# Performance work log

Measured on AMD Instinct MI355X. Metric: run time of the kernel, lower is better.

## Reference

```python
import jax, jax.numpy as jnp
import numpy as np

B, N, C = 16, 577, 768
H = 12
D = C // H
HID = C // 2
TEMP_MIN, TEMP_MAX = 0.5, 3.0


def setup_inputs() -> dict:
    key = jax.random.key(0)
    ks = jax.random.split(key, 8)
    s = 0.02
    return {
        "x": jax.random.normal(ks[0], (B, N, C), dtype=jnp.float32),
        "qkv_w": jax.random.normal(ks[1], (C, 3 * C), dtype=jnp.float32) * s,
        "proj_w": jax.random.normal(ks[2], (C, C), dtype=jnp.float32) * s,
        "proj_b": jnp.zeros((C,), dtype=jnp.float32),
        "t_w1": jax.random.normal(ks[3], (C, HID), dtype=jnp.float32) * s,
        "t_b1": jnp.zeros((HID,), dtype=jnp.float32),
        "t_w2": jax.random.normal(ks[4], (HID, 1), dtype=jnp.float32) * s,
        "t_b2": jnp.zeros((1,), dtype=jnp.float32),
    }


def reference(x, qkv_w, proj_w, proj_b, t_w1, t_b1, t_w2, t_b2):
    b, n, c = x.shape
    scale = D ** -0.5
    # instance-wise temperature from CLS token: (B, 1)
    cls = x[:, 0]
    h = jax.nn.relu(cls @ t_w1 + t_b1)
    t_norm = jax.nn.sigmoid(h @ t_w2 + t_b2)
    temperature = TEMP_MIN + (TEMP_MAX - TEMP_MIN) * t_norm  # (B, 1)

    qkv = (x @ qkv_w).reshape(b, n, 3, H, D)
    q = qkv[:, :, 0].transpose(0, 2, 1, 3)  # (B, H, N, D)
    k = qkv[:, :, 1].transpose(0, 2, 1, 3)
    v = qkv[:, :, 2].transpose(0, 2, 1, 3)

    attn = jnp.einsum('bhqd,bhkd->bhqk', q, k) * scale
    attn = attn / temperature[:, :, None, None]  # (B,1,1,1) broadcast
    attn = jax.nn.softmax(attn, axis=-1)
    out = jnp.einsum('bhqk,bhkd->bhqd', attn, v)
    out = out.transpose(0, 2, 1, 3).reshape(b, n, c)
    return out @ proj_w + proj_b
```

## Files before the change

kernel.cpp:

```cpp
#include <hip/hip_runtime.h>
#include <hip/hip_bf16.h>
#include <stdint.h>

typedef unsigned short u16;
typedef unsigned int   u32;
typedef uint64_t       u64;

using f32x4  = __attribute__((ext_vector_type(4))) float;
using bf16x8 = __attribute__((ext_vector_type(8))) short;

__device__ __forceinline__ u16 f2bf(float f){
  u32 x = __builtin_bit_cast(u32, f);
  x = x + 0x7fffu + ((x >> 16) & 1u);
  return (u16)(x >> 16);
}

__device__ __forceinline__ void gload16(const void* g, void* l){
  __builtin_amdgcn_global_load_lds(
      (const __attribute__((address_space(1))) void*)g,
      (__attribute__((address_space(3))) void*)l, 16, 0, 0);
}

__device__ __forceinline__ bf16x8 mkfrag(uint2 h0, uint2 h1){
  union { bf16x8 v; u32 u[4]; } f;
  f.u[0]=h0.x; f.u[1]=h0.y; f.u[2]=h1.x; f.u[3]=h1.y;
  return f.v;
}

__global__ void convx(const float* __restrict__ in, u16* __restrict__ out, int n4){
  for (int i = blockIdx.x*256 + threadIdx.x; i < n4; i += gridDim.x*256){
    float4 v = ((const float4*)in)[i];
    ushort4 o;
    o.x = f2bf(v.x); o.y = f2bf(v.y); o.z = f2bf(v.z); o.w = f2bf(v.w);
    ((ushort4*)out)[i] = o;
  }
}

__global__ __launch_bounds__(256) void wtrans(const float* __restrict__ in,
                                              u16* __restrict__ out, int K, int N){
  __shared__ float tile[32][33];
  const int t = threadIdx.x;
  const int n0 = blockIdx.x*32, k0 = blockIdx.y*32;
  const int r = t >> 3, c4 = (t & 7)*4;
  const float4 v = *(const float4*)(in + (u64)(k0 + r)*N + n0 + c4);
  tile[r][c4+0]=v.x; tile[r][c4+1]=v.y; tile[r][c4+2]=v.z; tile[r][c4+3]=v.w;
  __syncthreads();
  ushort4 o;
  o.x = f2bf(tile[c4+0][r]); o.y = f2bf(tile[c4+1][r]);
  o.z = f2bf(tile[c4+2][r]); o.w = f2bf(tile[c4+3][r]);
  *(ushort4*)(out + (u64)(n0 + r)*K + k0 + c4) = o;
}

__global__ __launch_bounds__(384) void temp_kernel(
    const float* __restrict__ x, const float* __restrict__ w1,
    const float* __restrict__ b1, const float* __restrict__ w2,
    const float* __restrict__ b2, float* __restrict__ lsc){
  const int b = blockIdx.x, t = threadIdx.x;
  __shared__ float cls[768];
  __shared__ float part[6];
  const float* xr = x + (u64)b*577*768;
  cls[t] = xr[t]; cls[t+384] = xr[t+384];
  __syncthreads();
  float h0 = 0.f, h1 = 0.f, h2 = 0.f, h3 = 0.f;
  for (int i = 0; i < 768; i += 4){
    h0 = fmaf(cls[i+0], w1[(u64)(i+0)*384 + t], h0);
    h1 = fmaf(cls[i+1], w1[(u64)(i+1)*384 + t], h1);
    h2 = fmaf(cls[i+2], w1[(u64)(i+2)*384 + t], h2);
    h3 = fmaf(cls[i+3], w1[(u64)(i+3)*384 + t], h3);
  }
  float hacc = fmaxf((h0 + h1) + (h2 + h3) + b1[t], 0.f);
  float v = hacc * w2[t];
  #pragma unroll
  for (int off = 1; off < 64; off <<= 1) v += __shfl_xor(v, off);
  if ((t & 63) == 0) part[t >> 6] = v;
  __syncthreads();
  if (t == 0){
    float s2 = b2[0];
    for (int i = 0; i < 6; i++) s2 += part[i];
    float sig  = 1.f / (1.f + expf(-s2));
    float temp = 0.5f + 2.5f * sig;
    lsc[b] = 0.125f / temp;
  }
}

template<int OUTF>
__global__ __launch_bounds__(256, 2) void gemm_nt(
    const u16* __restrict__ A, const u16* __restrict__ Bm,
    void* __restrict__ Cout, const float* __restrict__ bias,
    const float* __restrict__ lsc, int M, int N){
  constexpr int K = 768;
  __shared__ u16 As[128*64];
  __shared__ u16 Bs[128*64];
  const int t = threadIdx.x, l = t & 63, w = t >> 6;
  const int bm = blockIdx.y*128, bn = blockIdx.x*128;
  const int wr = (w >> 1)*64, wc = (w & 1)*64;
  const int g = l >> 4, r16 = l & 15;

  f32x4 acc[4][4];
  #pragma unroll
  for (int i = 0; i < 4; i++)
    #pragma unroll
    for (int j = 0; j < 4; j++) acc[i][j] = (f32x4){0.f,0.f,0.f,0.f};

  const int srow = t >> 3;
  const int su   = (t & 7) ^ (srow & 7);
  const u16* gA[4]; const u16* gB[4];
  #pragma unroll
  for (int i = 0; i < 4; i++){
    int ra = bm + i*32 + srow; if (ra > M-1) ra = M-1;
    gA[i] = A  + (u64)ra*K + su*8;
    gB[i] = Bm + (u64)(bn + i*32 + srow)*K + su*8;
  }
  u16* lA = As + t*8;
  u16* lB = Bs + t*8;

  for (int kt = 0; kt < K; kt += 64){
    #pragma unroll
    for (int i = 0; i < 4; i++) gload16(gA[i] + kt, lA + i*2048);
    #pragma unroll
    for (int i = 0; i < 4; i++) gload16(gB[i] + kt, lB + i*2048);
    __syncthreads();
    #pragma unroll
    for (int s = 0; s < 2; s++){
      const int c   = s*4 + (g >> 1);
      const int off = (g & 1)*4;
      bf16x8 af[4], bfr[4];
      #pragma unroll
      for (int m = 0; m < 4; m++){
        const int R = wr + m*16 + r16;
        const int i1 = R*64 + ((c ^ (R & 7))*8) + off;
        af[m] = mkfrag(*(const uint2*)(As + i1), *(const uint2*)(As + (i1 ^ 16)));
      }
      #pragma unroll
      for (int n = 0; n < 4; n++){
        const int R = wc + n*16 + r16;
        const int i1 = R*64 + ((c ^ (R & 7))*8) + off;
        bfr[n] = mkfrag(*(const uint2*)(Bs + i1), *(const uint2*)(Bs + (i1 ^ 16)));
      }
      #pragma unroll
      for (int m = 0; m < 4; m++)
        #pragma unroll
        for (int n = 0; n < 4; n++)
          acc[m][n] = __builtin_amdgcn_mfma_f32_16x16x32_bf16(af[m], bfr[n], acc[m][n], 0, 0, 0);
    }
    __syncthreads();
  }
  const int row0 = bm + wr + g*4;
  const int col0 = bn + wc + r16;
  const bool isQ = (OUTF == 2) && (bn < 768);
  #pragma unroll
  for (int m = 0; m < 4; m++){
    #pragma unroll
    for (int rr = 0; rr < 4; rr++){
      const int row = row0 + m*16 + rr;
      if (row < M){
        float qs = 1.0f;
        if (isQ) qs = lsc[row/577];
        #pragma unroll
        for (int n = 0; n < 4; n++){
          const int col = col0 + n*16;
          const float v = acc[m][n][rr];
          if (OUTF == 1) ((float*)Cout)[(u64)row*N + col] = v + bias[col];
          else           ((u16*)Cout)[(u64)row*N + col]  = f2bf(v*qs);
        }
      }
    }
  }
}

__global__ __launch_bounds__(256, 2) void attn_kernel(
    const u16* __restrict__ qkv, u16* __restrict__ aout){
  const u32 lid  = blockIdx.x;
  const u32 orig = (lid & 7u)*240u + (lid >> 3);
  const int qt = orig % 10u;
  const u32 bh = orig / 10u;
  const int h  = bh % 12u;
  const int b  = bh / 12u;
  const int t = threadIdx.x, w = t >> 6, l = t & 63;
  const int g = l >> 4, r16 = l & 15;
  __shared__ u16 Ks[2][64*64];
  __shared__ u16 Vt[2][64*64];
  const u16* base = qkv + (u64)b*577*2304 + (u64)h*64;

  int qn = qt*64 + w*16 + r16; if (qn > 576) qn = 576;
  bf16x8 qf[2];
  {
    const u16* qr = base + (u64)qn*2304;
    #pragma unroll
    for (int s = 0; s < 2; s++)
      qf[s] = mkfrag(*(const uint2*)(qr + s*32 + g*4),
                     *(const uint2*)(qr + s*32 + g*4 + 16));
  }
  float m_run = -1e30f, l_run = 0.f;
  f32x4 oacc[4];
  #pragma unroll
  for (int i = 0; i < 4; i++) oacc[i] = (f32x4){0,0,0,0};

  const int srcb = (l & 48) | (((l >> 4) & 3)*4);

  const int srow = t >> 3;
  const int su   = (t & 7) ^ (srow & 7);
  const u16* pK = base + 768  + (u64)srow*2304 + su*8;
  const int kr0 = (t >> 3)*2;
  const u16* pV = base + 1536 + (u64)kr0*2304 + (t & 7)*8;
  u32 vtoff[8];
  #pragma unroll
  for (int j = 0; j < 8; j++){
    const int d = (t & 7)*8 + j;
    const int key = (d ^ (d >> 3)) & 7;
    vtoff[j] = d*64 + (((kr0 >> 3) ^ key)*8) + (kr0 & 7);
  }

  uint4 vr0, vr1;
  gload16(pK,            &Ks[0][0] + t*8);
  gload16(pK + 32*2304,  &Ks[0][0] + t*8 + 2048);
  vr0 = *(const uint4*)pV;
  vr1 = *(const uint4*)(pV + 2304);
  pK += 64*2304; pV += 64*2304;
  {
    const u16* e0 = (const u16*)&vr0;
    const u16* e1 = (const u16*)&vr1;
    #pragma unroll
    for (int j = 0; j < 8; j++)
      *(u32*)(&Vt[0][0] + vtoff[j]) = (u32)e0[j] | ((u32)e1[j] << 16);
  }
  __syncthreads();

  for (int kt = 0; kt < 9; kt++){
    const int cur = kt & 1, nb = cur ^ 1;
    u16* ksc = &Ks[cur][0];
    u16* vtc = &Vt[cur][0];
    if (kt < 8){
      gload16(pK,           &Ks[nb][0] + t*8);
      gload16(pK + 32*2304, &Ks[nb][0] + t*8 + 2048);
      vr0 = *(const uint4*)pV;
      vr1 = *(const uint4*)(pV + 2304);
      pK += 64*2304; pV += 64*2304;
    }

    f32x4 sacc[4];
    #pragma unroll
    for (int i = 0; i < 4; i++) sacc[i] = (f32x4){0,0,0,0};
    #pragma unroll
    for (int fn = 0; fn < 4; fn++){
      const int kr = fn*16 + r16;
      const int kk = kr & 7;
      const u16* rowp = ksc + kr*64 + (g & 1)*4;
      #pragma unroll
      for (int s = 0; s < 2; s++){
        const int b0 = (4*s + (g >> 1)) ^ kk;
        sacc[fn] = __builtin_amdgcn_mfma_f32_16x16x32_bf16(
            mkfrag(*(const uint2*)(rowp + b0*8), *(const uint2*)(rowp + (b0 ^ 2)*8)),
            qf[s], sacc[fn], 0, 0, 0);
      }
    }
    float mx = sacc[0][0];
    #pragma unroll
    for (int fn = 0; fn < 4; fn++)
      #pragma unroll
      for (int rr = 0; rr < 4; rr++) mx = fmaxf(mx, sacc[fn][rr]);
    mx = fmaxf(mx, __shfl_xor(mx, 16));
    mx = fmaxf(mx, __shfl_xor(mx, 32));
    if (!__all(mx - m_run <= 8.f)){
      const float nm = fmaxf(m_run, mx);
      const float corr = __expf(m_run - nm);
      l_run *= corr;
      float corrO[4];
      #pragma unroll
      for (int rr = 0; rr < 4; rr++) corrO[rr] = __shfl(corr, srcb + rr);
      #pragma unroll
      for (int df = 0; df < 4; df++)
        #pragma unroll
        for (int rr = 0; rr < 4; rr++) oacc[df][rr] *= corrO[rr];
      m_run = nm;
    }
    float pf[4][4];
    float rs = 0.f;
    #pragma unroll
    for (int fn = 0; fn < 4; fn++)
      #pragma unroll
      for (int rr = 0; rr < 4; rr++){
        const float p = __expf(sacc[fn][rr] - m_run);
        rs += p;
        pf[fn][rr] = p;
      }
    rs += __shfl_xor(rs, 16);
    rs += __shfl_xor(rs, 32);
    l_run += rs;
    #pragma unroll
    for (int s = 0; s < 2; s++){
      union { bf16x8 v; u32 u[4]; } pa;
      asm("v_cvt_pk_bf16_f32 %0, %1, %2" : "=v"(pa.u[0]) : "v"(pf[2*s][0]),   "v"(pf[2*s][1]));
      asm("v_cvt_pk_bf16_f32 %0, %1, %2" : "=v"(pa.u[1]) : "v"(pf[2*s][2]),   "v"(pf[2*s][3]));
      asm("v_cvt_pk_bf16_f32 %0, %1, %2" : "=v"(pa.u[2]) : "v"(pf[2*s+1][0]), "v"(pf[2*s+1][1]));
      asm("v_cvt_pk_bf16_f32 %0, %1, %2" : "=v"(pa.u[3]) : "v"(pf[2*s+1][2]), "v"(pf[2*s+1][3]));
      #pragma unroll
      for (int df = 0; df < 4; df++){
        const int vd = df*16 + r16;
        const int vk = (vd ^ (vd >> 3)) & 7;
        const u16* vrp = vtc + vd*64 + (g & 1)*4;
        const int c0 = (4*s + (g >> 1)) ^ vk;
        const bf16x8 vf = mkfrag(*(const uint2*)(vrp + c0*8),
                                 *(const uint2*)(vrp + (c0 ^ 2)*8));
        oacc[df] = __builtin_amdgcn_mfma_f32_16x16x32_bf16(pa.v, vf, oacc[df], 0, 0, 0);
      }
    }
    if (kt < 8){
      const u16* e0 = (const u16*)&vr0;
      const u16* e1 = (const u16*)&vr1;
      u16* vtn = &Vt[nb][0];
      #pragma unroll
      for (int j = 0; j < 8; j++)
        *(u32*)(vtn + vtoff[j]) = (u32)e0[j] | ((u32)e1[j] << 16);
      __syncthreads();
    }
  }

  {
    const u16* kr576 = base + 768 + (u64)576*2304;
    float s576 = 0.f;
    #pragma unroll
    for (int s = 0; s < 2; s++){
      const uint2 k0 = *(const uint2*)(kr576 + s*32 + g*4);
      const uint2 k1 = *(const uint2*)(kr576 + s*32 + g*4 + 16);
      union { bf16x8 v; u32 u[4]; } qq; qq.v = qf[s];
      const u32 ku[4] = {k0.x, k0.y, k1.x, k1.y};
      #pragma unroll
      for (int j = 0; j < 4; j++){
        const float ql = __builtin_bit_cast(float, qq.u[j] << 16);
        const float qh = __builtin_bit_cast(float, qq.u[j] & 0xffff0000u);
        const float kl = __builtin_bit_cast(float, ku[j] << 16);
        const float kh = __builtin_bit_cast(float, ku[j] & 0xffff0000u);
        s576 = fmaf(ql, kl, s576);
        s576 = fmaf(qh, kh, s576);
      }
    }
    s576 += __shfl_xor(s576, 16);
    s576 += __shfl_xor(s576, 32);
    if (!__all(s576 - m_run <= 8.f)){
      const float nm = fmaxf(m_run, s576);
      const float corr = __expf(m_run - nm);
      l_run *= corr;
      float corrO[4];
      #pragma unroll
      for (int rr = 0; rr < 4; rr++) corrO[rr] = __shfl(corr, srcb + rr);
      #pragma unroll
      for (int df = 0; df < 4; df++)
        #pragma unroll
        for (int rr = 0; rr < 4; rr++) oacc[df][rr] *= corrO[rr];
      m_run = nm;
    }
    const float p576 = __expf(s576 - m_run);
    l_run += p576;
    float pbr[4];
    #pragma unroll
    for (int rr = 0; rr < 4; rr++) pbr[rr] = __shfl(p576, srcb + rr);
    const u16* v576 = base + 1536 + (u64)576*2304;
    #pragma unroll
    for (int df = 0; df < 4; df++){
      const float vv = __builtin_bit_cast(float, (u32)v576[df*16 + r16] << 16);
      #pragma unroll
      for (int rr = 0; rr < 4; rr++)
        oacc[df][rr] = fmaf(pbr[rr], vv, oacc[df][rr]);
    }
  }

  float lO[4];
  #pragma unroll
  for (int rr = 0; rr < 4; rr++) lO[rr] = __shfl(l_run, srcb + rr);
  #pragma unroll
  for (int df = 0; df < 4; df++){
    const int d = df*16 + r16;
    #pragma unroll
    for (int rr = 0; rr < 4; rr++){
      const int n = qt*64 + w*16 + g*4 + rr;
      if (n <= 576){
        const float v = oacc[df][rr] / lO[rr];
        aout[(u64)(b*577 + n)*768 + h*64 + d] = f2bf(v);
      }
    }
  }
}

extern "C" void kernel_launch(void* const* d_in, const int* in_sizes, int n_in,
                              void* d_out, int out_size, void* d_ws, size_t ws_size,
                              hipStream_t stream){
  const float* x      = (const float*)d_in[0];
  const float* qkv_w  = (const float*)d_in[1];
  const float* proj_w = (const float*)d_in[2];
  const float* proj_b = (const float*)d_in[3];
  const float* t_w1   = (const float*)d_in[4];
  const float* t_b1   = (const float*)d_in[5];
  const float* t_w2   = (const float*)d_in[6];
  const float* t_b2   = (const float*)d_in[7];

  const u64 off_xb  = 256;
  const u64 off_qwT = off_xb  + 14180352ull;
  const u64 off_pwT = off_qwT + 3538944ull;
  const u64 off_qkv = off_pwT + 1179648ull;
  const u64 need    = off_qkv + 42541056ull;
  if (ws_size < need) return;

  char* ws  = (char*)d_ws;
  float* lsc = (float*)ws;
  u16* xb   = (u16*)(ws + off_xb);
  u16* qwT  = (u16*)(ws + off_qwT);
  u16* pwT  = (u16*)(ws + off_pwT);
  u16* qkv  = (u16*)(ws + off_qkv);
  u16* ao   = xb;

  convx<<<1024, 256, 0, stream>>>(x, xb, (16*577*768)/4);
  wtrans<<<dim3(2304/32, 768/32), 256, 0, stream>>>(qkv_w, qwT, 768, 2304);
  wtrans<<<dim3(768/32, 768/32), 256, 0, stream>>>(proj_w, pwT, 768, 768);
  temp_kernel<<<16, 384, 0, stream>>>(x, t_w1, t_b1, t_w2, t_b2, lsc);
  gemm_nt<2><<<dim3(2304/128, 73), 256, 0, stream>>>(xb, qwT, qkv, nullptr, lsc, 9232, 2304);
  attn_kernel<<<1920, 256, 0, stream>>>(qkv, ao);
  gemm_nt<1><<<dim3(768/128, 73), 256, 0, stream>>>(ao, pwT, d_out, proj_b, nullptr, 9232, 768);
}
```

Before: 238.3 us.

## Fuse prep kernels into one launch and remap GEMM tiles per XCD

Folds the x-to-bf16 conversion, the two weight transposes and the temperature MLP into a single prep kernel that dispatches on block index, cutting three kernel launches and their gaps. Separately, both GEMMs move to a 1D grid whose block ids are remapped so consecutive output tiles land on the same XCD, which should improve L2 reuse of the A/B panels. The temperature path now runs with 256 threads handling two hidden units each. The fused kernel carries the shared-memory footprint of every branch, and the temperature blocks are few and serial, so they may form a tail.

Result: faster. 232.9 us (-2.2%).

```diff
diff --git a/kernel.cpp b/kernel.cpp
--- a/kernel.cpp
+++ b/kernel.cpp
@@ -27,59 +27,75 @@
   return f.v;
 }
 
-__global__ void convx(const float* __restrict__ in, u16* __restrict__ out, int n4){
-  for (int i = blockIdx.x*256 + threadIdx.x; i < n4; i += gridDim.x*256){
-    float4 v = ((const float4*)in)[i];
+__global__ __launch_bounds__(256) void prep_kernel(
+    const float* __restrict__ x, const float* __restrict__ qkv_w,
+    const float* __restrict__ proj_w,
+    const float* __restrict__ t_w1, const float* __restrict__ t_b1,
+    const float* __restrict__ t_w2, const float* __restrict__ t_b2,
+    u16* __restrict__ xb, u16* __restrict__ qwT, u16* __restrict__ pwT,
+    float* __restrict__ lsc){
+  __shared__ float tile[32][33];
+  __shared__ float cls[768];
+  __shared__ float part[4];
+  const int bid = blockIdx.x, t = threadIdx.x;
+
+  if (bid < 1024){
+    const int n4 = 16*577*768/4;
+    for (int i = bid*256 + t; i < n4; i += 1024*256){
+      float4 v = ((const float4*)x)[i];
+      ushort4 o;
+      o.x = f2bf(v.x); o.y = f2bf(v.y); o.z = f2bf(v.z); o.w = f2bf(v.w);
+      ((ushort4*)xb)[i] = o;
+    }
+  } else if (bid < 3328){
+    const bool isQ = bid < 2752;
+    const int r    = isQ ? (bid - 1024) : (bid - 2752);
+    const int nbx  = isQ ? 72 : 24;
+    const int N    = isQ ? 2304 : 768;
+    const float* in = isQ ? qkv_w : proj_w;
+    u16* out        = isQ ? qwT   : pwT;
+    const int n0 = (r % nbx)*32, k0 = (r / nbx)*32;
+    const int rr = t >> 3, c4 = (t & 7)*4;
+    const float4 v = *(const float4*)(in + (u64)(k0 + rr)*N + n0 + c4);
+    tile[rr][c4+0]=v.x; tile[rr][c4+1]=v.y; tile[rr][c4+2]=v.z; tile[rr][c4+3]=v.w;
+    __syncthreads();
     ushort4 o;
-    o.x = f2bf(v.x); o.y = f2bf(v.y); o.z = f2bf(v.z); o.w = f2bf(v.w);
-    ((ushort4*)out)[i] = o;
-  }
-}
-
-__global__ __launch_bounds__(256) void wtrans(const float* __restrict__ in,
-                                              u16* __restrict__ out, int K, int N){
-  __shared__ float tile[32][33];
-  const int t = threadIdx.x;
-  const int n0 = blockIdx.x*32, k0 = blockIdx.y*32;
-  const int r = t >> 3, c4 = (t & 7)*4;
-  const float4 v = *(const float4*)(in + (u64)(k0 + r)*N + n0 + c4);
-  tile[r][c4+0]=v.x; tile[r][c4+1]=v.y; tile[r][c4+2]=v.z; tile[r][c4+3]=v.w;
-  __syncthreads();
-  ushort4 o;
-  o.x = f2bf(tile[c4+0][r]); o.y = f2bf(tile[c4+1][r]);
-  o.z = f2bf(tile[c4+2][r]); o.w = f2bf(tile[c4+3][r]);
-  *(ushort4*)(out + (u64)(n0 + r)*K + k0 + c4) = o;
-}
-
-__global__ __launch_bounds__(384) void temp_kernel(
-    const float* __restrict__ x, const float* __restrict__ w1,
-    const float* __restrict__ b1, const float* __restrict__ w2,
-    const float* __restrict__ b2, float* __restrict__ lsc){
-  const int b = blockIdx.x, t = threadIdx.x;
-  __shared__ float cls[768];
-  __shared__ float part[6];
-  const float* xr = x + (u64)b*577*768;
-  cls[t] = xr[t]; cls[t+384] = xr[t+384];
-  __syncthreads();
-  float h0 = 0.f, h1 = 0.f, h2 = 0.f, h3 = 0.f;
-  for (int i = 0; i < 768; i += 4){
-    h0 = fmaf(cls[i+0], w1[(u64)(i+0)*384 + t], h0);
-    h1 = fmaf(cls[i+1], w1[(u64)(i+1)*384 + t], h1);
-    h2 = fmaf(cls[i+2], w1[(u64)(i+2)*384 + t], h2);
-    h3 = fmaf(cls[i+3], w1[(u64)(i+3)*384 + t], h3);
-  }
-  float hacc = fmaxf((h0 + h1) + (h2 + h3) + b1[t], 0.f);
-  float v = hacc * w2[t];
-  #pragma unroll
-  for (int off = 1; off < 64; off <<= 1) v += __shfl_xor(v, off);
-  if ((t & 63) == 0) part[t >> 6] = v;
-  __syncthreads();
-  if (t == 0){
-    float s2 = b2[0];
-    for (int i = 0; i < 6; i++) s2 += part[i];
-    float sig  = 1.f / (1.f + expf(-s2));
-    float temp = 0.5f + 2.5f * sig;
-    lsc[b] = 0.125f / temp;
+    o.x = f2bf(tile[c4+0][rr]); o.y = f2bf(tile[c4+1][rr]);
+    o.z = f2bf(tile[c4+2][rr]); o.w = f2bf(tile[c4+3][rr]);
+    *(ushort4*)(out + (u64)(n0 + rr)*768 + k0 + c4) = o;
+  } else {
+    const int b = bid - 3328;
+    const float* xr = x + (u64)b*577*768;
+    cls[t] = xr[t]; cls[t+256] = xr[t+256]; cls[t+512] = xr[t+512];
+    __syncthreads();
+    float v = 0.f;
+    if (t < 192){
+      const int j = t*2;
+      float a0=0.f, a1=0.f, b0=0.f, b1=0.f;
+      for (int i = 0; i < 768; i += 2){
+        const float2 w0 = *(const float2*)(t_w1 + (u64)i*384 + j);
+        const float2 w1v = *(const float2*)(t_w1 + (u64)(i+1)*384 + j);
+        a0 = fmaf(cls[i],   w0.x,  a0);
+        b0 = fmaf(cls[i],   w0.y,  b0);
+        a1 = fmaf(cls[i+1], w1v.x, a1);
+        b1 = fmaf(cls[i+1], w1v.y, b1);
+      }
+      const float2 bb = *(const float2*)(t_b1 + j);
+      const float2 ww = *(const float2*)(t_w2 + j);
+      const float hA = fmaxf(a0 + a1 + bb.x, 0.f);
+      const float hB = fmaxf(b0 + b1 + bb.y, 0.f);
+      v = hA*ww.x + hB*ww.y;
+    }
+    #pragma unroll
+    for (int off = 1; off < 64; off <<= 1) v += __shfl_xor(v, off);
+    if ((t & 63) == 0) part[t >> 6] = v;
+    __syncthreads();
+    if (t == 0){
+      const float s2 = part[0] + part[1] + part[2] + part[3] + t_b2[0];
+      const float sig  = 1.f / (1.f + expf(-s2));
+      const float temp = 0.5f + 2.5f * sig;
+      lsc[b] = 0.125f / temp;
+    }
   }
 }
 
@@ -87,12 +103,16 @@
 __global__ __launch_bounds__(256, 2) void gemm_nt(
     const u16* __restrict__ A, const u16* __restrict__ Bm,
     void* __restrict__ Cout, const float* __restrict__ bias,
-    const float* __restrict__ lsc, int M, int N){
+    const float* __restrict__ lsc, int M, int N, int nbx){
   constexpr int K = 768;
   __shared__ u16 As[128*64];
   __shared__ u16 Bs[128*64];
   const int t = threadIdx.x, l = t & 63, w = t >> 6;
-  const int bm = blockIdx.y*128, bn = blockIdx.x*128;
+  const u32 nwg = gridDim.x;
+  const u32 qc = nwg >> 3, rc = nwg & 7;
+  const u32 xcd = blockIdx.x & 7, lin = blockIdx.x >> 3;
+  const u32 wg = (xcd < rc ? xcd*(qc+1) : rc*(qc+1) + (xcd-rc)*qc) + lin;
+  const int bm = (int)(wg / (u32)nbx)*128, bn = (int)(wg % (u32)nbx)*128;
   const int wr = (w >> 1)*64, wc = (w & 1)*64;
   const int g = l >> 4, r16 = l & 15;
 
@@ -409,11 +429,9 @@
   u16* qkv  = (u16*)(ws + off_qkv);
   u16* ao   = xb;
 
-  convx<<<1024, 256, 0, stream>>>(x, xb, (16*577*768)/4);
-  wtrans<<<dim3(2304/32, 768/32), 256, 0, stream>>>(qkv_w, qwT, 768, 2304);
-  wtrans<<<dim3(768/32, 768/32), 256, 0, stream>>>(proj_w, pwT, 768, 768);
-  temp_kernel<<<16, 384, 0, stream>>>(x, t_w1, t_b1, t_w2, t_b2, lsc);
-  gemm_nt<2><<<dim3(2304/128, 73), 256, 0, stream>>>(xb, qwT, qkv, nullptr, lsc, 9232, 2304);
+  prep_kernel<<<3344, 256, 0, stream>>>(x, qkv_w, proj_w, t_w1, t_b1, t_w2, t_b2,
+                                        xb, qwT, pwT, lsc);
+  gemm_nt<2><<<1314, 256, 0, stream>>>(xb, qwT, qkv, nullptr, lsc, 9232, 2304, 18);
   attn_kernel<<<1920, 256, 0, stream>>>(qkv, ao);
-  gemm_nt<1><<<dim3(768/128, 73), 256, 0, stream>>>(ao, pwT, d_out, proj_b, nullptr, 9232, 768);
-}
+  gemm_nt<1><<<438, 256, 0, stream>>>(ao, pwT, d_out, proj_b, nullptr, 9232, 768, 6);
+}
```
